# Kernel tuning notes

Measured on AMD Instinct MI355X. Metric: run time of the kernel, lower is better.

## Reference

```python
import jax, jax.numpy as jnp
import numpy as np

N = 20000      # nodes
E = 640000     # edges (avg degree 32)
F_X = 256      # node feature dim
F_E = 256      # edge feature dim
D = 2048       # hidden width
D_OUT = 512    # final Linear out_channels
EPS = 1e-5     # torch LayerNorm default eps


def _glorot_like(k, fan_in, fan_out):
    # torch nn.Linear default: U(-1/sqrt(fan_in), 1/sqrt(fan_in))
    lim = (1.0 / fan_in) ** 0.5
    return jax.random.uniform(k, (fan_in, fan_out), minval=-lim, maxval=lim, dtype=jnp.float32)


def setup_inputs() -> dict:
    key = jax.random.key(0)
    ks = jax.random.split(key, 8)
    return {
        "x": jax.random.normal(ks[0], (N, F_X), dtype=jnp.float32),
        "edge_index": jax.random.randint(ks[1], (2, E), 0, N),
        "edge_attr": jax.random.normal(ks[2], (E, F_E), dtype=jnp.float32),
        # u = (u, nb, eb) in the original; unused by this setup (no conv1d/GraphNorm)
        "u_counts": jnp.array([N], dtype=jnp.int32),
        "nb": jnp.zeros((N,), dtype=jnp.int32),
        "eb": jnp.zeros((E,), dtype=jnp.int32),
        # learned params per setup
        "W1": _glorot_like(ks[3], F_X + F_E, D), "b1": jnp.zeros((D,), jnp.float32),
        "W3": _glorot_like(ks[4], D, D),         "b3": jnp.zeros((D,), jnp.float32),
        "ln_g": jnp.ones((D,), jnp.float32),      "ln_b": jnp.zeros((D,), jnp.float32),
        "W6": _glorot_like(ks[5], D + F_X + F_E, D), "b6": jnp.zeros((D,), jnp.float32),
        "W8": _glorot_like(ks[6], D, D_OUT),      "b8": jnp.zeros((D_OUT,), jnp.float32),
    }


def reference(x, edge_index, edge_attr, u_counts, nb, eb,
              W1, b1, W3, b3, ln_g, ln_b, W6, b6, W8, b8):
    # scatter_mean(edge_attr, col, dim=0, dim_size=N)
    col = edge_index[1]
    seg_sum = jax.ops.segment_sum(edge_attr, col, num_segments=N)           # [N, F_E]
    cnt = jax.ops.segment_sum(jnp.ones((edge_attr.shape[0],), edge_attr.dtype),
                              col, num_segments=N)                           # [N]
    agg = seg_sum / jnp.maximum(cnt, 1.0)[:, None]                           # mean; 0 for empty slots

    h0 = jnp.concatenate([agg, x], axis=1)                                   # [N, F_E+F_X]
    # layer 1-2: Linear -> ReLU
    h2 = jax.nn.relu(h0 @ W1 + b1)                                           # [N, D]
    # layer 3-4: Linear -> ReLU
    h4 = jax.nn.relu(h2 @ W3 + b3)                                           # [N, D]
    # layer 5: LayerNorm (affine)
    mu = jnp.mean(h4, axis=-1, keepdims=True)
    var = jnp.var(h4, axis=-1, keepdims=True)
    h5 = (h4 - mu) * jax.lax.rsqrt(var + EPS) * ln_g + ln_b
    # layer 6-7: Linear over concat(h5, merge_in) -> ReLU  (skip connection)
    h7 = jax.nn.relu(jnp.concatenate([h5, h0], axis=1) @ W6 + b6)            # [N, D]
    # layer 8: Linear -> out[-1]
    return h7 @ W8 + b8                                                      # [N, D_OUT]
```

## Files before the change

### kernel.cpp

```cpp
#include <hip/hip_runtime.h>

typedef unsigned short ushort_t;
typedef __attribute__((ext_vector_type(4))) float f32x4;
typedef __attribute__((ext_vector_type(8))) __bf16 bf16x8;
typedef __attribute__((ext_vector_type(8))) unsigned short u16x8;
typedef __attribute__((ext_vector_type(4))) unsigned short u16x4;

__device__ __forceinline__ unsigned short f2bf(float f) {
  union { float f; unsigned int u; } v; v.f = f;
  unsigned int u = v.u;
  u += 0x7fffu + ((u >> 16) & 1u);
  return (unsigned short)(u >> 16);
}

__device__ __forceinline__ float bf2f(unsigned short h) {
  union { unsigned int u; float f; } v; v.u = ((unsigned int)h) << 16;
  return v.f;
}

__device__ __forceinline__ void gload16(ushort_t* lds, const ushort_t* g) {
  __builtin_amdgcn_global_load_lds(
      (const __attribute__((address_space(1))) unsigned int*)g,
      (__attribute__((address_space(3))) unsigned int*)lds, 16, 0, 0);
}

__global__ __launch_bounds__(256)
void transpose_w(const float* __restrict__ in, ushort_t* __restrict__ out, int R, int C) {
  __shared__ float tile[32][33];
  const int t = threadIdx.x;
  const int tx = t & 31, ty = t >> 5;
  const int r0 = blockIdx.x * 32, c0 = blockIdx.y * 32;
#pragma unroll
  for (int i = 0; i < 4; ++i)
    tile[ty + 8 * i][tx] = in[(size_t)(r0 + ty + 8 * i) * C + c0 + tx];
  __syncthreads();
#pragma unroll
  for (int i = 0; i < 4; ++i)
    out[(size_t)(c0 + ty + 8 * i) * R + r0 + tx] = f2bf(tile[tx][ty + 8 * i]);
}

__global__ __launch_bounds__(256)
void count_edges(const int* __restrict__ col, int* __restrict__ cnt, int E) {
  int i = blockIdx.x * 256 + threadIdx.x;
  if (i < E) atomicAdd(&cnt[col[i]], 1);
}

__global__ __launch_bounds__(1024)
void prefix_kernel(const int* __restrict__ cnt, int* __restrict__ start,
                   int* __restrict__ cursor, int N) {
  const int t = threadIdx.x;
  const int chunk = (N + 1023) >> 10;
  const int base = t * chunk;
  int s = 0;
  for (int j = 0; j < chunk; ++j) {
    int i = base + j;
    s += (i < N) ? cnt[i] : 0;
  }
  const int lane = t & 63, wv = t >> 6;
  int scan = s;
#pragma unroll
  for (int o = 1; o < 64; o <<= 1) {
    int up = __shfl_up(scan, o);
    if (lane >= o) scan += up;
  }
  __shared__ int wsum[16];
  if (lane == 63) wsum[wv] = scan;
  __syncthreads();
  if (t == 0) {
    int acc = 0;
#pragma unroll
    for (int i2 = 0; i2 < 16; ++i2) { int v = wsum[i2]; wsum[i2] = acc; acc += v; }
  }
  __syncthreads();
  int run = wsum[wv] + (scan - s);
  for (int j = 0; j < chunk; ++j) {
    int i = base + j;
    if (i < N) {
      start[i] = run; cursor[i] = run;
      run += cnt[i];
    }
  }
}

__global__ __launch_bounds__(256)
void fill_csr(const int* __restrict__ col, int* __restrict__ cursor,
              int* __restrict__ eids, int E) {
  int i = blockIdx.x * 256 + threadIdx.x;
  if (i < E) {
    int p = atomicAdd(&cursor[col[i]], 1);
    eids[p] = i;
  }
}

__global__ __launch_bounds__(256)
void gather_mean(const float* __restrict__ eattr, const int* __restrict__ start,
                 const int* __restrict__ deg, const int* __restrict__ eids,
                 const float* __restrict__ x, ushort_t* __restrict__ hcat, int N) {
  const int row = blockIdx.x;
  const int t = threadIdx.x;
  const int w = t >> 6, l = t & 63;
  const int s = start[row], d = deg[row];
  const float4* ea4 = (const float4*)eattr;
  float4 sum = make_float4(0.f, 0.f, 0.f, 0.f);
  for (int i = w; i < d; i += 4) {
    int e = eids[s + i];
    float4 v = ea4[(size_t)e * 64 + l];
    sum.x += v.x; sum.y += v.y; sum.z += v.z; sum.w += v.w;
  }
  __shared__ float4 part[4][64];
  part[w][l] = sum;
  __syncthreads();
  hcat[(size_t)row * 2560 + 2304 + t] = f2bf(x[(size_t)row * 256 + t]);
  if (w == 0) {
    float4 a = part[0][l], b = part[1][l], c = part[2][l], dd = part[3][l];
    const float inv = 1.f / fmaxf((float)d, 1.f);
    u16x4 o;
    o[0] = f2bf((a.x + b.x + c.x + dd.x) * inv);
    o[1] = f2bf((a.y + b.y + c.y + dd.y) * inv);
    o[2] = f2bf((a.z + b.z + c.z + dd.z) * inv);
    o[3] = f2bf((a.w + b.w + c.w + dd.w) * inv);
    *(u16x4*)(hcat + (size_t)row * 2560 + 2048 + l * 4) = o;
  }
}

__global__ __launch_bounds__(256)
void ln_kernel(ushort_t* __restrict__ hcat, const float* __restrict__ g,
               const float* __restrict__ b) {
  const int row = blockIdx.x;
  const int t = threadIdx.x;
  ushort_t* p = hcat + (size_t)row * 2560 + t * 8;
  u16x8 raw = *(const u16x8*)p;
  float vv[8];
#pragma unroll
  for (int j = 0; j < 8; ++j) vv[j] = bf2f(raw[j]);
  float s = 0.f, ss = 0.f;
#pragma unroll
  for (int j = 0; j < 8; ++j) { s += vv[j]; ss += vv[j] * vv[j]; }
#pragma unroll
  for (int o = 32; o > 0; o >>= 1) {
    s += __shfl_xor(s, o);
    ss += __shfl_xor(ss, o);
  }
  __shared__ float red[8];
  int w = t >> 6, l = t & 63;
  if (l == 0) { red[w] = s; red[4 + w] = ss; }
  __syncthreads();
  s = red[0] + red[1] + red[2] + red[3];
  ss = red[4] + red[5] + red[6] + red[7];
  const float mu = s * (1.f / 2048.f);
  const float var = ss * (1.f / 2048.f) - mu * mu;
  const float rs = rsqrtf(var + 1e-5f);
  float4 g0 = *(const float4*)(g + t * 8);
  float4 g1 = *(const float4*)(g + t * 8 + 4);
  float4 b0 = *(const float4*)(b + t * 8);
  float4 b1 = *(const float4*)(b + t * 8 + 4);
  float gg[8] = {g0.x, g0.y, g0.z, g0.w, g1.x, g1.y, g1.z, g1.w};
  float bb[8] = {b0.x, b0.y, b0.z, b0.w, b1.x, b1.y, b1.z, b1.w};
  u16x8 o8;
#pragma unroll
  for (int j = 0; j < 8; ++j) o8[j] = f2bf((vv[j] - mu) * rs * gg[j] + bb[j]);
  *(u16x8*)p = o8;
}


#define SBAR() do { __builtin_amdgcn_sched_barrier(0); \
                    __builtin_amdgcn_s_barrier(); \
                    __builtin_amdgcn_sched_barrier(0); } while (0)

template <int RELU, int OUTBF>
__global__ __launch_bounds__(512, 4)
void gemm128(const ushort_t* __restrict__ A, int lda,
             const ushort_t* __restrict__ Bt,
             const float* __restrict__ bias,
             void* __restrict__ Cout, int ldc, int M, int K) {
  __shared__ __align__(16) ushort_t smem[36864];
  char* sb = (char*)smem;
  const int t = threadIdx.x;

  const int nct = gridDim.x;
  const int nwg = nct * gridDim.y;
  const int flat = blockIdx.y * nct + blockIdx.x;
  const int xcd = flat & 7, loc = flat >> 3;
  const int q = nwg >> 3, r = nwg & 7;
  const int swz = (xcd < r ? xcd * (q + 1) : r * (q + 1) + (xcd - r) * q) + loc;
  const int row0 = (swz / nct) * 128;
  const int col0 = (swz % nct) * 256;

  const int wid = t >> 6, l = t & 63;
  const int wr = wid >> 2, wc = wid & 3;
  const int lr = l & 15, lk = l >> 4;

  const int srow = t >> 2;
  const int scol = ((t & 3) ^ ((t >> 2) & 3)) << 3;
  int ar = row0 + srow; if (ar > M - 1) ar = M - 1;
  const ushort_t* pa  = A + (size_t)ar * lda + scol;
  const ushort_t* pb0 = Bt + (size_t)(col0 + srow) * K + scol;
  const ushort_t* pb1 = pb0 + (size_t)128 * K;
  const int tb = t * 16;

  const int sx = ((lk ^ (lr & 3)) << 4);
  const int arow = (wr * 64 + lr) * 64 + sx;
  const int brow = 8192 + (wc * 64 + lr) * 64 + sx;

  f32x4 acc[4][4] = {};

  const int nk = K >> 5;

  {
    const int k1 = (nk > 1) ? 32 : 0;
    gload16((ushort_t*)(sb + 8192 + tb), pb0);
    gload16((ushort_t*)(sb + 16384 + tb), pb1);
    gload16((ushort_t*)(sb + 0 + tb), pa);
    gload16((ushort_t*)(sb + 24576 + 8192 + tb), pb0 + k1);
    gload16((ushort_t*)(sb + 24576 + 16384 + tb), pb1 + k1);
    gload16((ushort_t*)(sb + 24576 + 0 + tb), pa + k1);
  }
  asm volatile("s_waitcnt vmcnt(3)" ::: "memory");
  SBAR();

  int cO = 0, sO = 49152;
  for (int k = 0; k < nk; ++k) {
    const int kc2 = ((k + 2 < nk) ? k + 2 : nk - 1) << 5;

    bf16x8 a[4], b[4];
#pragma unroll
    for (int m = 0; m < 4; ++m)
      a[m] = *(const bf16x8*)(sb + cO + arow + m * 1024);
#pragma unroll
    for (int n = 0; n < 4; ++n)
      b[n] = *(const bf16x8*)(sb + cO + brow + n * 1024);
    gload16((ushort_t*)(sb + sO + 8192 + tb), pb0 + kc2);
    gload16((ushort_t*)(sb + sO + 16384 + tb), pb1 + kc2);
    gload16((ushort_t*)(sb + sO + 0 + tb), pa + kc2);

    __builtin_amdgcn_s_setprio(1);
#pragma unroll
    for (int m = 0; m < 4; ++m)
#pragma unroll
      for (int n = 0; n < 4; ++n)
        acc[m][n] = __builtin_amdgcn_mfma_f32_16x16x32_bf16(b[n], a[m], acc[m][n], 0, 0, 0);
    __builtin_amdgcn_s_setprio(0);

    asm volatile("s_waitcnt vmcnt(3)" ::: "memory");
    SBAR();

    cO = (cO == 49152) ? 0 : cO + 24576;
    sO = (sO == 49152) ? 0 : sO + 24576;
  }
  asm volatile("s_waitcnt vmcnt(0)" ::: "memory");

#pragma unroll
  for (int mi = 0; mi < 4; ++mi) {
    const int orow = row0 + wr * 64 + mi * 16 + lr;
    if (orow < M) {
#pragma unroll
      for (int nj = 0; nj < 4; ++nj) {
        const int cb = col0 + wc * 64 + nj * 16 + lk * 4;
        const float4 bv = *(const float4*)(bias + cb);
        f32x4 v = acc[mi][nj];
        float o0 = v[0] + bv.x, o1 = v[1] + bv.y, o2 = v[2] + bv.z, o3 = v[3] + bv.w;
        if (RELU) {
          o0 = fmaxf(o0, 0.f); o1 = fmaxf(o1, 0.f);
          o2 = fmaxf(o2, 0.f); o3 = fmaxf(o3, 0.f);
        }
        if (OUTBF) {
          u16x4 o;
          o[0] = f2bf(o0); o[1] = f2bf(o1); o[2] = f2bf(o2); o[3] = f2bf(o3);
          *(u16x4*)((ushort_t*)Cout + (size_t)orow * ldc + cb) = o;
        } else {
          float4 ov = make_float4(o0, o1, o2, o3);
          *(float4*)((float*)Cout + (size_t)orow * ldc + cb) = ov;
        }
      }
    }
  }
}

extern "C" void kernel_launch(void* const* d_in, const int* in_sizes, int n_in,
                              void* d_out, int out_size, void* d_ws, size_t ws_size,
                              hipStream_t stream) {
  (void)n_in; (void)out_size; (void)ws_size;
  const float* x     = (const float*)d_in[0];
  const int*   eidx  = (const int*)d_in[1];
  const float* eattr = (const float*)d_in[2];
  const float* W1 = (const float*)d_in[6];
  const float* b1 = (const float*)d_in[7];
  const float* W3 = (const float*)d_in[8];
  const float* b3 = (const float*)d_in[9];
  const float* lng = (const float*)d_in[10];
  const float* lnb = (const float*)d_in[11];
  const float* W6 = (const float*)d_in[12];
  const float* b6 = (const float*)d_in[13];
  const float* W8 = (const float*)d_in[14];
  const float* b8 = (const float*)d_in[15];

  const int N = in_sizes[0] / 256;
  const int E = in_sizes[2] / 256;
  const int* col = eidx + E;

  char* ws = (char*)d_ws;
  size_t off = 0;
  ushort_t* hcat = (ushort_t*)(ws + off);  off += (size_t)N * 2560 * 2;
  ushort_t* h2   = (ushort_t*)(ws + off);  off += (size_t)N * 2048 * 2;
  ushort_t* W1t = (ushort_t*)(ws + off);   off += (size_t)2048 * 512 * 2;
  ushort_t* W3t = (ushort_t*)(ws + off);   off += (size_t)2048 * 2048 * 2;
  ushort_t* W6t = (ushort_t*)(ws + off);   off += (size_t)2048 * 2560 * 2;
  ushort_t* W8t = (ushort_t*)(ws + off);   off += (size_t)512 * 2048 * 2;
  int* deg    = (int*)(ws + off);  off += (size_t)N * 4;
  int* startp = (int*)(ws + off);  off += (size_t)N * 4;
  int* cursor = (int*)(ws + off);  off += (size_t)N * 4;
  int* eids   = (int*)(ws + off);  off += (size_t)E * 4;

  hipMemsetAsync(deg, 0, (size_t)N * 4, stream);

  transpose_w<<<dim3(512 / 32, 2048 / 32), 256, 0, stream>>>(W1, W1t, 512, 2048);
  transpose_w<<<dim3(2048 / 32, 2048 / 32), 256, 0, stream>>>(W3, W3t, 2048, 2048);
  transpose_w<<<dim3(2560 / 32, 2048 / 32), 256, 0, stream>>>(W6, W6t, 2560, 2048);
  transpose_w<<<dim3(2048 / 32, 512 / 32), 256, 0, stream>>>(W8, W8t, 2048, 512);

  count_edges<<<(E + 255) / 256, 256, 0, stream>>>(col, deg, E);
  prefix_kernel<<<1, 1024, 0, stream>>>(deg, startp, cursor, N);
  fill_csr<<<(E + 255) / 256, 256, 0, stream>>>(col, cursor, eids, E);
  gather_mean<<<N, 256, 0, stream>>>(eattr, startp, deg, eids, x, hcat, N);

  const int Mt = (N + 127) / 128;
  gemm128<1, 1><<<dim3(8, Mt), 512, 0, stream>>>(hcat + 2048, 2560, W1t, b1, h2, 2048, N, 512);
  gemm128<1, 1><<<dim3(8, Mt), 512, 0, stream>>>(h2, 2048, W3t, b3, hcat, 2560, N, 2048);
  ln_kernel<<<N, 256, 0, stream>>>(hcat, lng, lnb);
  gemm128<1, 1><<<dim3(8, Mt), 512, 0, stream>>>(hcat, 2560, W6t, b6, h2, 2048, N, 2560);
  gemm128<0, 0><<<dim3(2, Mt), 512, 0, stream>>>(h2, 2048, W8t, b8, (float*)d_out, 512, N, 2048);
}
```

Before: 843.9 us.

## Load A tiles directly to registers, stage only B through LDS

The A operand is now loaded straight from global memory into registers with per-lane addressing and double-buffered across two register sets, instead of being staged through LDS. Only the B tile goes through a triple-buffered LDS ring, and the k loop is unrolled by two. This shrinks LDS use and drops the A LDS reads, which could allow more occupancy and cut LDS bandwidth. The cost is more register pressure and uncoalesced 16-byte A loads that rely on the cache, and the nk-odd case and the vmcnt accounting are fragile.

New measurement: 1.839 ms. 2.18x slower.

```diff
diff --git a/kernel.cpp b/kernel.cpp
--- a/kernel.cpp
+++ b/kernel.cpp
@@ -173,7 +173,7 @@
              const ushort_t* __restrict__ Bt,
              const float* __restrict__ bias,
              void* __restrict__ Cout, int ldc, int M, int K) {
-  __shared__ __align__(16) ushort_t smem[36864];
+  __shared__ __align__(16) ushort_t smem[24576];
   char* sb = (char*)smem;
   const int t = threadIdx.x;
 
@@ -192,60 +192,84 @@
 
   const int srow = t >> 2;
   const int scol = ((t & 3) ^ ((t >> 2) & 3)) << 3;
-  int ar = row0 + srow; if (ar > M - 1) ar = M - 1;
-  const ushort_t* pa  = A + (size_t)ar * lda + scol;
   const ushort_t* pb0 = Bt + (size_t)(col0 + srow) * K + scol;
   const ushort_t* pb1 = pb0 + (size_t)128 * K;
   const int tb = t * 16;
 
   const int sx = ((lk ^ (lr & 3)) << 4);
-  const int arow = (wr * 64 + lr) * 64 + sx;
-  const int brow = 8192 + (wc * 64 + lr) * 64 + sx;
+  const int brow = (wc * 64 + lr) * 64 + sx;
+
+  const char* Ab = (const char*)A;
+  unsigned int av[4];
+#pragma unroll
+  for (int m = 0; m < 4; ++m) {
+    int rr = row0 + wr * 64 + m * 16 + lr;
+    if (rr > M - 1) rr = M - 1;
+    av[m] = (unsigned int)rr * (unsigned int)(lda * 2) + (unsigned int)(lk * 16);
+  }
 
   f32x4 acc[4][4] = {};
+  bf16x8 a[4], a2[4], b[4];
 
   const int nk = K >> 5;
 
-  {
-    const int k1 = (nk > 1) ? 32 : 0;
-    gload16((ushort_t*)(sb + 8192 + tb), pb0);
-    gload16((ushort_t*)(sb + 16384 + tb), pb1);
-    gload16((ushort_t*)(sb + 0 + tb), pa);
-    gload16((ushort_t*)(sb + 24576 + 8192 + tb), pb0 + k1);
-    gload16((ushort_t*)(sb + 24576 + 16384 + tb), pb1 + k1);
-    gload16((ushort_t*)(sb + 24576 + 0 + tb), pa + k1);
-  }
-  asm volatile("s_waitcnt vmcnt(3)" ::: "memory");
+#pragma unroll
+  for (int m = 0; m < 4; ++m) a[m] = *(const bf16x8*)(Ab + av[m]);
+  gload16((ushort_t*)(sb + tb), pb0);
+  gload16((ushort_t*)(sb + 8192 + tb), pb1);
+#pragma unroll
+  for (int m = 0; m < 4; ++m) a2[m] = *(const bf16x8*)(Ab + av[m] + 64);
+  gload16((ushort_t*)(sb + 16384 + tb), pb0 + 32);
+  gload16((ushort_t*)(sb + 16384 + 8192 + tb), pb1 + 32);
+  asm volatile("s_waitcnt vmcnt(6)" ::: "memory");
   SBAR();
 
-  int cO = 0, sO = 49152;
-  for (int k = 0; k < nk; ++k) {
-    const int kc2 = ((k + 2 < nk) ? k + 2 : nk - 1) << 5;
-
-    bf16x8 a[4], b[4];
-#pragma unroll
-    for (int m = 0; m < 4; ++m)
-      a[m] = *(const bf16x8*)(sb + cO + arow + m * 1024);
-#pragma unroll
-    for (int n = 0; n < 4; ++n)
-      b[n] = *(const bf16x8*)(sb + cO + brow + n * 1024);
-    gload16((ushort_t*)(sb + sO + 8192 + tb), pb0 + kc2);
-    gload16((ushort_t*)(sb + sO + 16384 + tb), pb1 + kc2);
-    gload16((ushort_t*)(sb + sO + 0 + tb), pa + kc2);
-
-    __builtin_amdgcn_s_setprio(1);
-#pragma unroll
-    for (int m = 0; m < 4; ++m)
+  int cO = 0;
+  for (int k = 0; k < nk; k += 2) {
+    {
+      const int kc = (k + 2 < nk) ? k + 2 : nk - 1;
+      const int sO = (cO == 0) ? 32768 : cO - 16384;
 #pragma unroll
       for (int n = 0; n < 4; ++n)
-        acc[m][n] = __builtin_amdgcn_mfma_f32_16x16x32_bf16(b[n], a[m], acc[m][n], 0, 0, 0);
-    __builtin_amdgcn_s_setprio(0);
-
-    asm volatile("s_waitcnt vmcnt(3)" ::: "memory");
-    SBAR();
-
-    cO = (cO == 49152) ? 0 : cO + 24576;
-    sO = (sO == 49152) ? 0 : sO + 24576;
+        b[n] = *(const bf16x8*)(sb + cO + brow + n * 1024);
+      gload16((ushort_t*)(sb + sO + tb), pb0 + kc * 32);
+      gload16((ushort_t*)(sb + sO + 8192 + tb), pb1 + kc * 32);
+      __builtin_amdgcn_s_setprio(1);
+#pragma unroll
+      for (int m = 0; m < 4; ++m)
+#pragma unroll
+        for (int n = 0; n < 4; ++n)
+          acc[m][n] = __builtin_amdgcn_mfma_f32_16x16x32_bf16(b[n], a[m], acc[m][n], 0, 0, 0);
+      __builtin_amdgcn_s_setprio(0);
+#pragma unroll
+      for (int m = 0; m < 4; ++m)
+        a[m] = *(const bf16x8*)(Ab + av[m] + kc * 64);
+      asm volatile("s_waitcnt vmcnt(6)" ::: "memory");
+      SBAR();
+      cO = (cO == 32768) ? 0 : cO + 16384;
+    }
+    {
+      const int kc = (k + 3 < nk) ? k + 3 : nk - 1;
+      const int sO = (cO == 0) ? 32768 : cO - 16384;
+#pragma unroll
+      for (int n = 0; n < 4; ++n)
+        b[n] = *(const bf16x8*)(sb + cO + brow + n * 1024);
+      gload16((ushort_t*)(sb + sO + tb), pb0 + kc * 32);
+      gload16((ushort_t*)(sb + sO + 8192 + tb), pb1 + kc * 32);
+      __builtin_amdgcn_s_setprio(1);
+#pragma unroll
+      for (int m = 0; m < 4; ++m)
+#pragma unroll
+        for (int n = 0; n < 4; ++n)
+          acc[m][n] = __builtin_amdgcn_mfma_f32_16x16x32_bf16(b[n], a2[m], acc[m][n], 0, 0, 0);
+      __builtin_amdgcn_s_setprio(0);
+#pragma unroll
+      for (int m = 0; m < 4; ++m)
+        a2[m] = *(const bf16x8*)(Ab + av[m] + kc * 64);
+      asm volatile("s_waitcnt vmcnt(6)" ::: "memory");
+      SBAR();
+      cO = (cO == 32768) ? 0 : cO + 16384;
+    }
   }
   asm volatile("s_waitcnt vmcnt(0)" ::: "memory");
 
```
